# Kernel optimization log

Hardware: AMD Instinct MI355X
Metric: run time of the kernel (lower is better)

## Reference

```python
import jax, jax.numpy as jnp
import numpy as np

# column-index constants for the node feature matrix and edge attributes
VM, VA, PG, QG, PD, QD = 0, 1, 2, 3, 4, 5
G_COL, B_COL = 0, 1

N_NODES = 100000
N_EDGES = 3200000
N_FEAT = 6


def setup_inputs() -> dict:
    key = jax.random.key(0)
    k1, k2, k3, k4, k5, k6 = jax.random.split(key, 6)
    pred = jax.random.normal(k1, (N_NODES, N_FEAT), dtype=jnp.float32)
    target = jax.random.normal(k2, (N_NODES, N_FEAT), dtype=jnp.float32)
    src = jax.random.randint(k3, (N_EDGES,), 0, N_NODES, dtype=jnp.int32)
    dst = jax.random.randint(k4, (N_EDGES,), 0, N_NODES, dtype=jnp.int32)
    edge_index = jnp.stack([src, dst], axis=0)
    edge_attr = jax.random.normal(k5, (N_EDGES, 2), dtype=jnp.float32)
    mask = jax.random.bernoulli(k6, 0.5, (N_NODES, N_FEAT))
    return {"pred": pred, "target": target, "edge_index": edge_index,
            "edge_attr": edge_attr, "mask": mask}


def reference(pred, target, edge_index, edge_attr, mask):
    # temp_pred[~mask] = target[~mask]
    tp = jnp.where(mask, pred, target)

    V_m = tp[:, VM]
    V_a = tp[:, VA]
    V = V_m * jnp.exp(1j * V_a)           # complex64 [N]
    V_conj = jnp.conj(V)

    # conj(Y_bus) entries on edges: G - jB
    Y_conj = edge_attr[:, G_COL] - 1j * edge_attr[:, B_COL]  # complex64 [E]

    row, col = edge_index[0], edge_index[1]
    # (Y_bus_conj @ V_conj)[i] = sum over edges (i,j) of conj(Y_ij) * conj(V_j)
    msg = Y_conj * V_conj[col]                               # gather-multiply [E]
    matvec = jax.ops.segment_sum(msg, row, num_segments=tp.shape[0])  # scatter-add [N]

    S_injection = V * matvec                                  # diag(V) @ (...)

    net_P = tp[:, PG] - tp[:, PD]
    net_Q = tp[:, QG] - tp[:, QD]
    diff = (net_P + 1j * net_Q) - S_injection

    loss = jnp.mean(jnp.abs(diff))
    real_loss = jnp.mean(jnp.abs(jnp.real(diff)))
    imag_loss = jnp.mean(jnp.abs(jnp.imag(diff)))
    return (loss, real_loss, imag_loss)
```

## Files before the change

### kernel.cpp

```cpp
#include <hip/hip_runtime.h>
#include <hip/hip_fp16.h>
#include <math.h>

constexpr int N_NODES = 100000;
constexpr int N_EDGES = 3200000;
constexpr int NF      = 6;

constexpr int BSHIFT  = 10;
constexpr int BNODES  = 1 << BSHIFT;
constexpr int NB      = (N_NODES + BNODES - 1) >> BSHIFT;
constexpr int CAP     = 33792;
constexpr int NSLICE  = 8;
constexpr int TILE    = 2048;
constexpr int EPT     = TILE / 256;
constexpr int NBLK_PART = (N_EDGES + TILE - 1) / TILE;
constexpr int VPREP_BLOCKS = (N_NODES + 255) / 256;

constexpr size_t OFF_V    = 0;
constexpr size_t OFF_CR   = OFF_V  + (size_t)N_NODES * 8;
constexpr size_t OFF_AT   = OFF_CR + (size_t)NB * CAP * 4;
constexpr size_t OFF_PART = OFF_AT + (size_t)NB * CAP * 4;
constexpr size_t OFF_CNT  = OFF_PART + (size_t)NB * NSLICE * BNODES * 8;
constexpr size_t WS_NEED  = OFF_CNT + 1024;

union F2U { float2 f; unsigned long long u; };

__global__ __launch_bounds__(256) void partition_edges(
        const int* __restrict__ row, const int* __restrict__ col,
        const float2* __restrict__ attr,
        const float* __restrict__ pred, const float* __restrict__ target,
        const unsigned char* __restrict__ mask,
        float2* __restrict__ v_out,
        unsigned int* __restrict__ gcur,
        unsigned int* __restrict__ colrow_g, unsigned int* __restrict__ attrh_g) {
    __shared__ unsigned int h[4][NB];
    __shared__ unsigned int cur[4][NB];
    __shared__ int wb[4][NB];
    __shared__ int dbase[NB];
    __shared__ unsigned int tot_s[NB];
    __shared__ unsigned int colrow_s[TILE];
    __shared__ unsigned int attrh_s[TILE];
    __shared__ unsigned char bkt_s[TILE];
    __shared__ int total_s;

    const int tid = threadIdx.x;
    const int w = tid >> 6;
    const int e0 = blockIdx.x * TILE;
    const int e_base = e0 + tid * EPT;
    const bool ok = e_base < N_EDGES;

    if (blockIdx.x < VPREP_BLOCKS) {
        int i = blockIdx.x * 256 + tid;
        if (i < N_NODES) {
            const int bb = i * NF;
            float vm = mask[bb + 0] ? pred[bb + 0] : target[bb + 0];
            float va = mask[bb + 1] ? pred[bb + 1] : target[bb + 1];
            float sn, cs;
            sincosf(va, &sn, &cs);
            v_out[i] = make_float2(vm * cs, vm * sn);
        }
    }

    for (int i = tid; i < 4 * NB; i += 256) {
        (&h[0][0])[i] = 0u;
        (&cur[0][0])[i] = 0u;
    }
    __syncthreads();

    int r[EPT];
    if (ok) {
        int4 ra = *(const int4*)(row + e_base);
        int4 rb = *(const int4*)(row + e_base + 4);
        r[0]=ra.x; r[1]=ra.y; r[2]=ra.z; r[3]=ra.w;
        r[4]=rb.x; r[5]=rb.y; r[6]=rb.z; r[7]=rb.w;
        #pragma unroll
        for (int k = 0; k < EPT; ++k)
            atomicAdd(&h[w][r[k] >> BSHIFT], 1u);
    }
    __syncthreads();

    if (tid < NB)
        tot_s[tid] = h[0][tid] + h[1][tid] + h[2][tid] + h[3][tid];
    __syncthreads();

    if (tid < NB) {
        int lbase = 0;
        for (int j = 0; j < tid; ++j) lbase += (int)tot_s[j];
        unsigned t0 = h[0][tid], t1 = h[1][tid], t2 = h[2][tid];
        unsigned tot = tot_s[tid];
        unsigned g = tot ? atomicAdd(&gcur[tid], tot) : 0u;
        dbase[tid] = (int)g - lbase;
        wb[0][tid] = lbase;
        wb[1][tid] = lbase + (int)t0;
        wb[2][tid] = lbase + (int)(t0 + t1);
        wb[3][tid] = lbase + (int)(t0 + t1 + t2);
        if (tid == NB - 1) total_s = lbase + (int)tot;
    }
    __syncthreads();

    if (ok) {
        int4 ca = *(const int4*)(col + e_base);
        int4 cb = *(const int4*)(col + e_base + 4);
        int c[EPT] = {ca.x, ca.y, ca.z, ca.w, cb.x, cb.y, cb.z, cb.w};
        float4 a0 = *(const float4*)(attr + e_base);
        float4 a1 = *(const float4*)(attr + e_base + 2);
        float4 a2 = *(const float4*)(attr + e_base + 4);
        float4 a3 = *(const float4*)(attr + e_base + 6);
        float gx[EPT] = {a0.x, a0.z, a1.x, a1.z, a2.x, a2.z, a3.x, a3.z};
        float gy[EPT] = {a0.y, a0.w, a1.y, a1.w, a2.y, a2.w, a3.y, a3.w};
        #pragma unroll
        for (int k = 0; k < EPT; ++k) {
            int rr = r[k];
            int b = rr >> BSHIFT;
            int slot = wb[w][b] + (int)atomicAdd(&cur[w][b], 1u);
            __half2 hh = __floats2half2_rn(gx[k], gy[k]);
            colrow_s[slot] = (unsigned)c[k] | ((unsigned)(rr & (BNODES - 1)) << 17);
            attrh_s[slot] = *reinterpret_cast<unsigned int*>(&hh);
            bkt_s[slot] = (unsigned char)b;
        }
    }
    __syncthreads();

    const int total = total_s;
    for (int j = tid; j < total; j += 256) {
        int b = (int)bkt_s[j];
        int g = dbase[b] + j;
        if (g < CAP) {
            size_t idx = (size_t)b * CAP + g;
            colrow_g[idx] = colrow_s[j];
            attrh_g[idx] = attrh_s[j];
        }
    }
}

__global__ __launch_bounds__(256) void accum_finalize(
        const unsigned int* __restrict__ gcur,
        const unsigned int* __restrict__ colrow,
        const unsigned int* __restrict__ attrh,
        unsigned long long* __restrict__ partials,
        unsigned int* __restrict__ sdone,
        float* __restrict__ sums,
        unsigned int* __restrict__ done_all,
        const float* __restrict__ pred,
        const float* __restrict__ target,
        const unsigned char* __restrict__ mask,
        const float2* __restrict__ v,
        float* __restrict__ out) {
    __shared__ float acc_re[BNODES];
    __shared__ float acc_im[BNODES];
    __shared__ unsigned int old_s;
    const int tid = threadIdx.x;
    const int b = blockIdx.x / NSLICE;
    const int s = blockIdx.x % NSLICE;
    int cnt = (int)min(gcur[b], (unsigned)CAP);
    for (int i = tid; i < BNODES; i += 256) { acc_re[i] = 0.f; acc_im[i] = 0.f; }
    __syncthreads();
    int per = (((cnt + NSLICE - 1) / NSLICE) + 1) & ~1;
    int st = s * per;
    int en = min(st + per, cnt);
    const unsigned int* crp = colrow + (size_t)b * CAP;
    const unsigned int* ahp = attrh + (size_t)b * CAP;
    #pragma unroll 2
    for (int j = st + 2 * tid; j < en; j += 512) {
        if (j + 1 < en) {
            uint2 cr = *(const uint2*)(crp + j);
            uint2 ah = *(const uint2*)(ahp + j);
            int c0 = (int)(cr.x & 0x1FFFFu), li0 = (int)(cr.x >> 17);
            int c1 = (int)(cr.y & 0x1FFFFu), li1 = (int)(cr.y >> 17);
            float2 vv0 = v[c0];
            float2 vv1 = v[c1];
            float2 gb0 = __half22float2(*reinterpret_cast<__half2*>(&ah.x));
            float2 gb1 = __half22float2(*reinterpret_cast<__half2*>(&ah.y));
            atomicAdd(&acc_re[li0], fmaf(gb0.x, vv0.x, -gb0.y * vv0.y));
            atomicAdd(&acc_im[li0], -fmaf(gb0.x, vv0.y, gb0.y * vv0.x));
            atomicAdd(&acc_re[li1], fmaf(gb1.x, vv1.x, -gb1.y * vv1.y));
            atomicAdd(&acc_im[li1], -fmaf(gb1.x, vv1.y, gb1.y * vv1.x));
        } else {
            unsigned cr = crp[j];
            unsigned ah = ahp[j];
            int c0 = (int)(cr & 0x1FFFFu), li0 = (int)(cr >> 17);
            float2 vv0 = v[c0];
            float2 gb0 = __half22float2(*reinterpret_cast<__half2*>(&ah));
            atomicAdd(&acc_re[li0], fmaf(gb0.x, vv0.x, -gb0.y * vv0.y));
            atomicAdd(&acc_im[li0], -fmaf(gb0.x, vv0.y, gb0.y * vv0.x));
        }
    }
    __syncthreads();
    unsigned long long* p = partials + ((size_t)b * NSLICE + s) * BNODES;
    for (int i = tid; i < BNODES; i += 256) {
        F2U cvt;
        cvt.f = make_float2(acc_re[i], acc_im[i]);
        __hip_atomic_store(&p[i], cvt.u, __ATOMIC_RELAXED, __HIP_MEMORY_SCOPE_AGENT);
    }
    asm volatile("s_waitcnt vmcnt(0)" ::: "memory");
    __syncthreads();
    if (tid == 0)
        old_s = __hip_atomic_fetch_add(&sdone[b], 1u, __ATOMIC_RELAXED,
                                       __HIP_MEMORY_SCOPE_AGENT);
    __syncthreads();
    if (old_s != (unsigned)(NSLICE - 1)) return;

    const unsigned long long* pb = partials + (size_t)b * NSLICE * BNODES;
    float a = 0.f, ar = 0.f, ai = 0.f;
    for (int li = tid; li < BNODES; li += 256) {
        int i = (b << BSHIFT) + li;
        if (i >= N_NODES) break;
        float mr = 0.f, mi = 0.f;
        #pragma unroll
        for (int s2 = 0; s2 < NSLICE; ++s2) {
            F2U cvt;
            cvt.u = __hip_atomic_load(&pb[(size_t)s2 * BNODES + li],
                                      __ATOMIC_RELAXED, __HIP_MEMORY_SCOPE_AGENT);
            mr += cvt.f.x; mi += cvt.f.y;
        }
        const int bb = i * NF;
        float pg = mask[bb + 2] ? pred[bb + 2] : target[bb + 2];
        float qg = mask[bb + 3] ? pred[bb + 3] : target[bb + 3];
        float pd = mask[bb + 4] ? pred[bb + 4] : target[bb + 4];
        float qd = mask[bb + 5] ? pred[bb + 5] : target[bb + 5];
        float netP = pg - pd;
        float netQ = qg - qd;
        float2 vv = v[i];
        float s_re = vv.x * mr - vv.y * mi;
        float s_im = vv.x * mi + vv.y * mr;
        float dre = netP - s_re;
        float dim = netQ - s_im;
        ar += fabsf(dre);
        ai += fabsf(dim);
        a  += sqrtf(dre * dre + dim * dim);
    }
    #pragma unroll
    for (int off = 32; off > 0; off >>= 1) {
        a  += __shfl_down(a,  off, 64);
        ar += __shfl_down(ar, off, 64);
        ai += __shfl_down(ai, off, 64);
    }
    __shared__ float red[3][4];
    int wave = tid >> 6;
    int lane = tid & 63;
    if (lane == 0) { red[0][wave] = a; red[1][wave] = ar; red[2][wave] = ai; }
    __syncthreads();
    if (tid == 0) {
        float r0 = atomicAdd(&sums[0], red[0][0] + red[0][1] + red[0][2] + red[0][3]);
        float r1 = atomicAdd(&sums[1], red[1][0] + red[1][1] + red[1][2] + red[1][3]);
        float r2 = atomicAdd(&sums[2], red[2][0] + red[2][1] + red[2][2] + red[2][3]);
        float chk = r0 + r1 + r2;
        if (chk == chk) {
            unsigned fin = atomicAdd(done_all, 1u);
            if (fin == (unsigned)(NB - 1)) {
                const float inv = 1.0f / (float)N_NODES;
                float t0 = atomicAdd(&sums[0], 0.f);
                float t1 = atomicAdd(&sums[1], 0.f);
                float t2 = atomicAdd(&sums[2], 0.f);
                __hip_atomic_store(&out[0], t0 * inv, __ATOMIC_RELAXED, __HIP_MEMORY_SCOPE_AGENT);
                __hip_atomic_store(&out[1], t1 * inv, __ATOMIC_RELAXED, __HIP_MEMORY_SCOPE_AGENT);
                __hip_atomic_store(&out[2], t2 * inv, __ATOMIC_RELAXED, __HIP_MEMORY_SCOPE_AGENT);
            }
        }
    }
}

__global__ void node_prep_fb(const float* __restrict__ pred,
                             const float* __restrict__ target,
                             const unsigned char* __restrict__ mask,
                             float2* __restrict__ v) {
    int i = blockIdx.x * blockDim.x + threadIdx.x;
    if (i >= N_NODES) return;
    const int b = i * NF;
    float vm = mask[b + 0] ? pred[b + 0] : target[b + 0];
    float va = mask[b + 1] ? pred[b + 1] : target[b + 1];
    float s, c;
    sincosf(va, &s, &c);
    v[i] = make_float2(vm * c, vm * s);
}

__global__ void edge_scatter_fb(const int* __restrict__ row,
                                const int* __restrict__ col,
                                const float2* __restrict__ attr,
                                const float2* __restrict__ v,
                                float2* __restrict__ mv) {
    int e = blockIdx.x * blockDim.x + threadIdx.x;
    if (e >= N_EDGES) return;
    int r = row[e];
    int c = col[e];
    float2 gb = attr[e];
    float2 vv = v[c];
    float mre = fmaf(gb.x, vv.x, -gb.y * vv.y);
    float mim = -fmaf(gb.x, vv.y, gb.y * vv.x);
    atomicAdd(&mv[r].x, mre);
    atomicAdd(&mv[r].y, mim);
}

__global__ void finalize_fb(const float* __restrict__ pred,
                            const float* __restrict__ target,
                            const unsigned char* __restrict__ mask,
                            const float2* __restrict__ v,
                            const float2* __restrict__ mv,
                            float* __restrict__ sums) {
    int i = blockIdx.x * blockDim.x + threadIdx.x;
    float a = 0.f, ar = 0.f, ai = 0.f;
    if (i < N_NODES) {
        const int b = i * NF;
        float pg = mask[b + 2] ? pred[b + 2] : target[b + 2];
        float qg = mask[b + 3] ? pred[b + 3] : target[b + 3];
        float pd = mask[b + 4] ? pred[b + 4] : target[b + 4];
        float qd = mask[b + 5] ? pred[b + 5] : target[b + 5];
        float netP = pg - pd;
        float netQ = qg - qd;
        float2 vv = v[i];
        float2 m = mv[i];
        float s_re = vv.x * m.x - vv.y * m.y;
        float s_im = vv.x * m.y + vv.y * m.x;
        float dre = netP - s_re;
        float dim = netQ - s_im;
        ar = fabsf(dre);
        ai = fabsf(dim);
        a  = sqrtf(dre * dre + dim * dim);
    }
    #pragma unroll
    for (int off = 32; off > 0; off >>= 1) {
        a  += __shfl_down(a,  off, 64);
        ar += __shfl_down(ar, off, 64);
        ai += __shfl_down(ai, off, 64);
    }
    __shared__ float red[3][4];
    int wave = threadIdx.x >> 6;
    int lane = threadIdx.x & 63;
    if (lane == 0) { red[0][wave] = a; red[1][wave] = ar; red[2][wave] = ai; }
    __syncthreads();
    if (threadIdx.x == 0) {
        atomicAdd(&sums[0], red[0][0] + red[0][1] + red[0][2] + red[0][3]);
        atomicAdd(&sums[1], red[1][0] + red[1][1] + red[1][2] + red[1][3]);
        atomicAdd(&sums[2], red[2][0] + red[2][1] + red[2][2] + red[2][3]);
    }
}

__global__ void write_out_fb(const float* __restrict__ sums, float* __restrict__ out) {
    if (threadIdx.x == 0 && blockIdx.x == 0) {
        const float inv = 1.0f / (float)N_NODES;
        out[0] = sums[0] * inv;
        out[1] = sums[1] * inv;
        out[2] = sums[2] * inv;
    }
}

extern "C" void kernel_launch(void* const* d_in, const int* in_sizes, int n_in,
                              void* d_out, int out_size, void* d_ws, size_t ws_size,
                              hipStream_t stream) {
    const float*         pred   = (const float*)d_in[0];
    const float*         target = (const float*)d_in[1];
    const int*           eidx   = (const int*)d_in[2];
    const float2*        attr   = (const float2*)d_in[3];
    const unsigned char* mask   = (const unsigned char*)d_in[4];
    float* out = (float*)d_out;

    const int* row = eidx;
    const int* col = eidx + N_EDGES;

    char* ws = (char*)d_ws;
    const int B = 256;

    if (ws_size >= WS_NEED) {
        float2*             v        = (float2*)(ws + OFF_V);
        unsigned int*       colrow_g = (unsigned int*)(ws + OFF_CR);
        unsigned int*       attrh_g  = (unsigned int*)(ws + OFF_AT);
        unsigned long long* partials = (unsigned long long*)(ws + OFF_PART);
        unsigned int*       gcur     = (unsigned int*)(ws + OFF_CNT);
        unsigned int*       sdone    = (unsigned int*)(ws + OFF_CNT + 512);
        float*              sums     = (float*)(ws + OFF_CNT + 912);
        unsigned int*       done_all = (unsigned int*)(ws + OFF_CNT + 928);

        hipMemsetAsync(ws + OFF_CNT, 0, 1024, stream);
        partition_edges<<<NBLK_PART, B, 0, stream>>>(row, col, attr,
                                                     pred, target, mask, v,
                                                     gcur, colrow_g, attrh_g);
        accum_finalize<<<NB * NSLICE, B, 0, stream>>>(gcur, colrow_g, attrh_g, partials,
                                                      sdone, sums, done_all,
                                                      pred, target, mask, v, out);
    } else {
        float2* v    = (float2*)ws;
        float2* mv   = (float2*)(ws + (size_t)N_NODES * 8);
        float*  sums = (float*)(ws + 2ull * N_NODES * 8);
        hipMemsetAsync(mv, 0, (size_t)N_NODES * 8 + 16, stream);
        node_prep_fb<<<(N_NODES + B - 1) / B, B, 0, stream>>>(pred, target, mask, v);
        edge_scatter_fb<<<(N_EDGES + B - 1) / B, B, 0, stream>>>(row, col, attr, v, mv);
        finalize_fb<<<(N_NODES + B - 1) / B, B, 0, stream>>>(pred, target, mask, v, mv, sums);
        write_out_fb<<<1, 64, 0, stream>>>(sums, out);
    }
}
```

Baseline: 189.4 us.

## Interleave edge records into uint2 and double accumulation slices with 4-wide loads

```diff
diff --git a/kernel.cpp b/kernel.cpp
--- a/kernel.cpp
+++ b/kernel.cpp
@@ -10,20 +10,25 @@
 constexpr int BNODES  = 1 << BSHIFT;
 constexpr int NB      = (N_NODES + BNODES - 1) >> BSHIFT;
 constexpr int CAP     = 33792;
-constexpr int NSLICE  = 8;
+constexpr int NSLICE  = 16;
 constexpr int TILE    = 2048;
 constexpr int EPT     = TILE / 256;
 constexpr int NBLK_PART = (N_EDGES + TILE - 1) / TILE;
 constexpr int VPREP_BLOCKS = (N_NODES + 255) / 256;
 
 constexpr size_t OFF_V    = 0;
-constexpr size_t OFF_CR   = OFF_V  + (size_t)N_NODES * 8;
-constexpr size_t OFF_AT   = OFF_CR + (size_t)NB * CAP * 4;
-constexpr size_t OFF_PART = OFF_AT + (size_t)NB * CAP * 4;
+constexpr size_t OFF_REC  = OFF_V  + (size_t)N_NODES * 8;
+constexpr size_t OFF_PART = OFF_REC + (size_t)NB * CAP * 8;
 constexpr size_t OFF_CNT  = OFF_PART + (size_t)NB * NSLICE * BNODES * 8;
 constexpr size_t WS_NEED  = OFF_CNT + 1024;
 
 union F2U { float2 f; unsigned long long u; };
+
+__device__ __forceinline__ float2 half2u_to_f2(unsigned u) {
+    __half2 h;
+    *reinterpret_cast<unsigned*>(&h) = u;
+    return __half22float2(h);
+}
 
 __global__ __launch_bounds__(256) void partition_edges(
         const int* __restrict__ row, const int* __restrict__ col,
@@ -32,14 +37,13 @@
         const unsigned char* __restrict__ mask,
         float2* __restrict__ v_out,
         unsigned int* __restrict__ gcur,
-        unsigned int* __restrict__ colrow_g, unsigned int* __restrict__ attrh_g) {
+        uint2* __restrict__ rec_g) {
     __shared__ unsigned int h[4][NB];
     __shared__ unsigned int cur[4][NB];
     __shared__ int wb[4][NB];
     __shared__ int dbase[NB];
     __shared__ unsigned int tot_s[NB];
-    __shared__ unsigned int colrow_s[TILE];
-    __shared__ unsigned int attrh_s[TILE];
+    __shared__ uint2 rec_s[TILE];
     __shared__ unsigned char bkt_s[TILE];
     __shared__ int total_s;
 
@@ -114,8 +118,9 @@
             int b = rr >> BSHIFT;
             int slot = wb[w][b] + (int)atomicAdd(&cur[w][b], 1u);
             __half2 hh = __floats2half2_rn(gx[k], gy[k]);
-            colrow_s[slot] = (unsigned)c[k] | ((unsigned)(rr & (BNODES - 1)) << 17);
-            attrh_s[slot] = *reinterpret_cast<unsigned int*>(&hh);
+            rec_s[slot] = make_uint2(
+                (unsigned)c[k] | ((unsigned)(rr & (BNODES - 1)) << 17),
+                *reinterpret_cast<unsigned int*>(&hh));
             bkt_s[slot] = (unsigned char)b;
         }
     }
@@ -125,18 +130,14 @@
     for (int j = tid; j < total; j += 256) {
         int b = (int)bkt_s[j];
         int g = dbase[b] + j;
-        if (g < CAP) {
-            size_t idx = (size_t)b * CAP + g;
-            colrow_g[idx] = colrow_s[j];
-            attrh_g[idx] = attrh_s[j];
-        }
+        if (g < CAP)
+            rec_g[(size_t)b * CAP + g] = rec_s[j];
     }
 }
 
 __global__ __launch_bounds__(256) void accum_finalize(
         const unsigned int* __restrict__ gcur,
-        const unsigned int* __restrict__ colrow,
-        const unsigned int* __restrict__ attrh,
+        const uint2* __restrict__ rec,
         unsigned long long* __restrict__ partials,
         unsigned int* __restrict__ sdone,
         float* __restrict__ sums,
@@ -155,35 +156,42 @@
     int cnt = (int)min(gcur[b], (unsigned)CAP);
     for (int i = tid; i < BNODES; i += 256) { acc_re[i] = 0.f; acc_im[i] = 0.f; }
     __syncthreads();
-    int per = (((cnt + NSLICE - 1) / NSLICE) + 1) & ~1;
+    int per = (((cnt + NSLICE - 1) / NSLICE) + 3) & ~3;
     int st = s * per;
     int en = min(st + per, cnt);
-    const unsigned int* crp = colrow + (size_t)b * CAP;
-    const unsigned int* ahp = attrh + (size_t)b * CAP;
-    #pragma unroll 2
-    for (int j = st + 2 * tid; j < en; j += 512) {
-        if (j + 1 < en) {
-            uint2 cr = *(const uint2*)(crp + j);
-            uint2 ah = *(const uint2*)(ahp + j);
-            int c0 = (int)(cr.x & 0x1FFFFu), li0 = (int)(cr.x >> 17);
-            int c1 = (int)(cr.y & 0x1FFFFu), li1 = (int)(cr.y >> 17);
-            float2 vv0 = v[c0];
-            float2 vv1 = v[c1];
-            float2 gb0 = __half22float2(*reinterpret_cast<__half2*>(&ah.x));
-            float2 gb1 = __half22float2(*reinterpret_cast<__half2*>(&ah.y));
-            atomicAdd(&acc_re[li0], fmaf(gb0.x, vv0.x, -gb0.y * vv0.y));
-            atomicAdd(&acc_im[li0], -fmaf(gb0.x, vv0.y, gb0.y * vv0.x));
-            atomicAdd(&acc_re[li1], fmaf(gb1.x, vv1.x, -gb1.y * vv1.y));
-            atomicAdd(&acc_im[li1], -fmaf(gb1.x, vv1.y, gb1.y * vv1.x));
-        } else {
-            unsigned cr = crp[j];
-            unsigned ah = ahp[j];
-            int c0 = (int)(cr & 0x1FFFFu), li0 = (int)(cr >> 17);
-            float2 vv0 = v[c0];
-            float2 gb0 = __half22float2(*reinterpret_cast<__half2*>(&ah));
-            atomicAdd(&acc_re[li0], fmaf(gb0.x, vv0.x, -gb0.y * vv0.y));
-            atomicAdd(&acc_im[li0], -fmaf(gb0.x, vv0.y, gb0.y * vv0.x));
-        }
+    const uint2* rp = rec + (size_t)b * CAP;
+    int j = st + 4 * tid;
+    for (; j + 3 < en; j += 1024) {
+        uint4 q0 = *(const uint4*)(rp + j);
+        uint4 q1 = *(const uint4*)(rp + j + 2);
+        int c0 = (int)(q0.x & 0x1FFFFu), li0 = (int)(q0.x >> 17);
+        int c1 = (int)(q0.z & 0x1FFFFu), li1 = (int)(q0.z >> 17);
+        int c2 = (int)(q1.x & 0x1FFFFu), li2 = (int)(q1.x >> 17);
+        int c3 = (int)(q1.z & 0x1FFFFu), li3 = (int)(q1.z >> 17);
+        float2 vv0 = v[c0];
+        float2 vv1 = v[c1];
+        float2 vv2 = v[c2];
+        float2 vv3 = v[c3];
+        float2 gb0 = half2u_to_f2(q0.y);
+        float2 gb1 = half2u_to_f2(q0.w);
+        float2 gb2 = half2u_to_f2(q1.y);
+        float2 gb3 = half2u_to_f2(q1.w);
+        atomicAdd(&acc_re[li0], fmaf(gb0.x, vv0.x, -gb0.y * vv0.y));
+        atomicAdd(&acc_im[li0], -fmaf(gb0.x, vv0.y, gb0.y * vv0.x));
+        atomicAdd(&acc_re[li1], fmaf(gb1.x, vv1.x, -gb1.y * vv1.y));
+        atomicAdd(&acc_im[li1], -fmaf(gb1.x, vv1.y, gb1.y * vv1.x));
+        atomicAdd(&acc_re[li2], fmaf(gb2.x, vv2.x, -gb2.y * vv2.y));
+        atomicAdd(&acc_im[li2], -fmaf(gb2.x, vv2.y, gb2.y * vv2.x));
+        atomicAdd(&acc_re[li3], fmaf(gb3.x, vv3.x, -gb3.y * vv3.y));
+        atomicAdd(&acc_im[li3], -fmaf(gb3.x, vv3.y, gb3.y * vv3.x));
+    }
+    for (; j < en; ++j) {
+        uint2 q = rp[j];
+        int c0 = (int)(q.x & 0x1FFFFu), li0 = (int)(q.x >> 17);
+        float2 vv0 = v[c0];
+        float2 gb0 = half2u_to_f2(q.y);
+        atomicAdd(&acc_re[li0], fmaf(gb0.x, vv0.x, -gb0.y * vv0.y));
+        atomicAdd(&acc_im[li0], -fmaf(gb0.x, vv0.y, gb0.y * vv0.x));
     }
     __syncthreads();
     unsigned long long* p = partials + ((size_t)b * NSLICE + s) * BNODES;
@@ -362,8 +370,7 @@
 
     if (ws_size >= WS_NEED) {
         float2*             v        = (float2*)(ws + OFF_V);
-        unsigned int*       colrow_g = (unsigned int*)(ws + OFF_CR);
-        unsigned int*       attrh_g  = (unsigned int*)(ws + OFF_AT);
+        uint2*              rec_g    = (uint2*)(ws + OFF_REC);
         unsigned long long* partials = (unsigned long long*)(ws + OFF_PART);
         unsigned int*       gcur     = (unsigned int*)(ws + OFF_CNT);
         unsigned int*       sdone    = (unsigned int*)(ws + OFF_CNT + 512);
@@ -373,8 +380,8 @@
         hipMemsetAsync(ws + OFF_CNT, 0, 1024, stream);
         partition_edges<<<NBLK_PART, B, 0, stream>>>(row, col, attr,
                                                      pred, target, mask, v,
-                                                     gcur, colrow_g, attrh_g);
-        accum_finalize<<<NB * NSLICE, B, 0, stream>>>(gcur, colrow_g, attrh_g, partials,
+                                                     gcur, rec_g);
+        accum_finalize<<<NB * NSLICE, B, 0, stream>>>(gcur, rec_g, partials,
                                                       sdone, sums, done_all,
                                                       pred, target, mask, v, out);
     } else {
```

Result: faster. 183.8 us (-2.9%).
